# Kernel optimization log

Hardware: AMD Instinct MI355X
Metric: run time of the kernel (lower is better)

## Reference

```python
import jax, jax.numpy as jnp
import numpy as np

N, E, F_IN, C, H12, H3, NCLS = 10000, 160000, 50, 256, 4, 6, 121


def gat_conv(x, src, dst, W, a_src, a_dst, b, heads, out_ch, concat, n):
    # x: [n, f_in]; W: [f_in, heads*out_ch]; a_*: [heads, out_ch]; src/dst: [e]
    h = (x @ W).reshape(n, heads, out_ch)
    # per-edge attention logits, LeakyReLU(0.2) as in PyG GATConv
    alpha = jax.nn.leaky_relu((h * a_src).sum(-1)[src] + (h * a_dst).sum(-1)[dst], 0.2)  # [e, heads]
    # segment softmax over incoming edges of each destination node
    amax = jax.ops.segment_max(alpha, dst, num_segments=n)
    ex = jnp.exp(alpha - amax[dst])
    denom = jax.ops.segment_sum(ex, dst, num_segments=n)
    w = ex / (denom[dst] + 1e-16)
    out = jax.ops.segment_sum(h[src] * w[..., None], dst, num_segments=n)  # [n, heads, out_ch]
    out = out.reshape(n, heads * out_ch) if concat else out.mean(axis=1)
    return out + b


def setup_inputs() -> dict:
    key = jax.random.key(0)
    ks = jax.random.split(key, 22)
    s = 0.05
    nrm = lambda k, shp: jax.random.normal(k, shp, jnp.float32) * s
    D = C * H12  # 1024
    return {
        "x": jax.random.normal(ks[0], (N, F_IN), jnp.float32),
        "edge_index": jax.random.randint(ks[1], (2, E), 0, N, dtype=jnp.int32),
        "W1": nrm(ks[2], (F_IN, H12 * C)), "a_src1": nrm(ks[3], (H12, C)), "a_dst1": nrm(ks[4], (H12, C)), "b1": jnp.zeros((H12 * C,), jnp.float32),
        "lW1": nrm(ks[5], (F_IN, D)), "lb1": jnp.zeros((D,), jnp.float32),
        "W2": nrm(ks[6], (D, H12 * C)), "a_src2": nrm(ks[7], (H12, C)), "a_dst2": nrm(ks[8], (H12, C)), "b2": jnp.zeros((H12 * C,), jnp.float32),
        "lW2": nrm(ks[9], (D, D)), "lb2": jnp.zeros((D,), jnp.float32),
        "W3": nrm(ks[10], (D, H3 * NCLS)), "a_src3": nrm(ks[11], (H3, NCLS)), "a_dst3": nrm(ks[12], (H3, NCLS)), "b3": jnp.zeros((NCLS,), jnp.float32),
        "lW3": nrm(ks[13], (D, NCLS)), "lb3": jnp.zeros((NCLS,), jnp.float32),
    }


def reference(x, edge_index, W1, a_src1, a_dst1, b1, lW1, lb1,
              W2, a_src2, a_dst2, b2, lW2, lb2,
              W3, a_src3, a_dst3, b3, lW3, lb3):
    n = x.shape[0]
    loop = jnp.arange(n, dtype=edge_index.dtype)  # self loops (PyG default)
    src = jnp.concatenate([edge_index[0], loop])
    dst = jnp.concatenate([edge_index[1], loop])
    h = jax.nn.elu(gat_conv(x, src, dst, W1, a_src1, a_dst1, b1, H12, C, True, n) + x @ lW1 + lb1)
    h = jax.nn.elu(gat_conv(h, src, dst, W2, a_src2, a_dst2, b2, H12, C, True, n) + h @ lW2 + lb2)
    return gat_conv(h, src, dst, W3, a_src3, a_dst3, b3, H3, NCLS, False, n) + h @ lW3 + lb3
```

## Files before the change

kernel.cpp:

```cpp
#include <hip/hip_runtime.h>
#include <cstdint>
#include <cstddef>

#define NN 10000
#define EE 160000
#define EN_ (EE + NN)
#define MPAD 10112
#define MT 79
#define CAP 128

typedef short s16x8 __attribute__((ext_vector_type(8)));
typedef float f32x4 __attribute__((ext_vector_type(4)));
typedef unsigned short u16;
typedef unsigned char u8;

__device__ __forceinline__ u16 f2bf(float f) {
  uint32_t u = __float_as_uint(f);
  uint32_t r = (u + 0x7fffu + ((u >> 16) & 1u)) >> 16;
  return (u16)r;
}
__device__ __forceinline__ float b2f_lo(uint32_t p) { return __uint_as_float(p << 16); }
__device__ __forceinline__ float b2f_hi(uint32_t p) { return __uint_as_float(p & 0xffff0000u); }
__device__ __forceinline__ float lrelu02(float x) { return x > 0.f ? x : 0.2f * x; }
__device__ __forceinline__ float eluf(float x) { return x > 0.f ? x : (__expf(x) - 1.f); }
__device__ __forceinline__ u8 f2fp8(float v) {
  v = fminf(fmaxf(v, -448.f), 448.f);
  return (u8)(__builtin_amdgcn_cvt_pk_fp8_f32(v, v, 0, false) & 0xff);
}

__global__ void k_count(const int* __restrict__ ei, int* __restrict__ cnt) {
  int e = blockIdx.x * blockDim.x + threadIdx.x;
  if (e >= EN_) return;
  int d = (e < EE) ? ei[EE + e] : (e - EE);
  atomicAdd(&cnt[d], 1);
}

__global__ __launch_bounds__(1024) void k_scan(const int* __restrict__ cnt, int* __restrict__ off) {
  __shared__ int sums[1024];
  int t = threadIdx.x;
  const int per = (NN + 1023) / 1024;
  int base = t * per;
  int local = 0;
  for (int j = 0; j < per; ++j) {
    int idx = base + j;
    if (idx < NN) local += cnt[idx];
  }
  sums[t] = local;
  __syncthreads();
  for (int s = 1; s < 1024; s <<= 1) {
    int v = (t >= s) ? sums[t - s] : 0;
    __syncthreads();
    sums[t] += v;
    __syncthreads();
  }
  int run = (t == 0) ? 0 : sums[t - 1];
  for (int j = 0; j < per; ++j) {
    int idx = base + j;
    if (idx < NN) { off[idx] = run; run += cnt[idx]; }
  }
  if (t == 1023) off[NN] = EN_;
}

__global__ void k_fill(const int* __restrict__ ei, const int* __restrict__ off,
                       int* __restrict__ cursor, int* __restrict__ csr_src) {
  int e = blockIdx.x * blockDim.x + threadIdx.x;
  if (e >= EN_) return;
  int s, d;
  if (e < EE) { s = ei[e]; d = ei[EE + e]; } else { s = d = e - EE; }
  int p = atomicAdd(&cursor[d], 1);
  csr_src[off[d] + p] = s;
}

#define PREP_BLOCKS 3490
__global__ __launch_bounds__(256) void k_prep(
    const float* __restrict__ x, u16* __restrict__ xb,
    const float* __restrict__ W1, const float* __restrict__ lW1,
    const float* __restrict__ W2, const float* __restrict__ lW2,
    const float* __restrict__ W3, const float* __restrict__ lW3,
    u16* __restrict__ wtc1, u16* __restrict__ wtc2, u16* __restrict__ wtc3,
    const float* __restrict__ lb1, const float* __restrict__ lb2,
    const float* __restrict__ lb3, float* __restrict__ fb,
    u16* __restrict__ bufX, int* __restrict__ cnt) {
  int b = blockIdx.x, t = threadIdx.x;
  if (b < 768) {
    const float* W; u16* Bt; int K, N, Kpad, nb, kb;
    if (b < 16)       { W = W1;  Bt = wtc1;                       K = 50;   N = 1024; Kpad = 64;   nb = b;      kb = 0; }
    else if (b < 32)  { W = lW1; Bt = wtc1 + (size_t)1024 * 64;   K = 50;   N = 1024; Kpad = 64;   nb = b - 16; kb = 0; }
    else if (b < 288) { int r = b - 32;  W = W2;  Bt = wtc2;                         K = 1024; N = 1024; Kpad = 1024; nb = r & 15; kb = r >> 4; }
    else if (b < 544) { int r = b - 288; W = lW2; Bt = wtc2 + (size_t)1024 * 1024;   K = 1024; N = 1024; Kpad = 1024; nb = r & 15; kb = r >> 4; }
    else if (b < 736) { int r = b - 544; W = W3;  Bt = wtc3;                         K = 1024; N = 726;  Kpad = 1024; nb = r % 12; kb = r / 12; }
    else              { int r = b - 736; W = lW3; Bt = wtc3 + (size_t)768 * 1024;    K = 1024; N = 121;  Kpad = 1024; nb = r & 1;  kb = r >> 1; }
    __shared__ float tile[64][65];
    int kbase = kb * 64, nbase = nb * 64;
    int nl = t & 63, kl0 = t >> 6;
#pragma unroll
    for (int j = 0; j < 16; ++j) {
      int k = kbase + kl0 + j * 4, n = nbase + nl;
      tile[kl0 + j * 4][nl] = (k < K && n < N) ? W[(size_t)k * N + n] : 0.f;
    }
    __syncthreads();
    int nr = t >> 2, kc = (t & 3) * 16;
    uint32_t pk[8];
#pragma unroll
    for (int j = 0; j < 8; ++j) {
      pk[j] = (uint32_t)f2bf(tile[kc + 2 * j][nr]) | ((uint32_t)f2bf(tile[kc + 2 * j + 1][nr]) << 16);
    }
    uint4* dst = (uint4*)(Bt + (size_t)(nbase + nr) * Kpad + kbase + kc);
    dst[0] = make_uint4(pk[0], pk[1], pk[2], pk[3]);
    dst[1] = make_uint4(pk[4], pk[5], pk[6], pk[7]);
  } else if (b < 3296) {
    int idx = (b - 768) * 256 + t;
    if (idx < MPAD * 64) {
      int m = idx >> 6, k = idx & 63;
      xb[idx] = f2bf((m < NN && k < 50) ? x[m * 50 + k] : 0.f);
    }
  } else if (b < 3352) {
    int idx = (b - 3296) * 256 + t;
    ((uint4*)(bufX + (size_t)NN * 1024))[idx] = make_uint4(0, 0, 0, 0);
  } else if (b < 3470) {
    int idx = (b - 3352) * 256 + t;
    if (idx < 3 * NN + 1) cnt[idx] = 0;
  } else {
    int idx = (b - 3470) * 256 + t;
    if (idx < 4992) {
      float v = 0.f;
      if (idx < 2048)      { if (idx >= 1024) v = lb1[idx - 1024]; }
      else if (idx < 4096) { int j = idx - 2048; if (j >= 1024) v = lb2[j - 1024]; }
      else                 { int j = idx - 4096; if (j >= 768 && j < 889) v = lb3[j - 768]; }
      fb[idx] = v;
    }
  }
}

template <int OUT_S_BF16>
__global__ __launch_bounds__(256) void k_gemm_fused(
    const u16* __restrict__ A, const u16* __restrict__ Bt,
    const float* __restrict__ fbias,
    u8* __restrict__ outH, int ldH,
    void* __restrict__ outS, int ldS, int nsplit, int nrealS,
    int M, int Kpad, int NS) {
  __shared__ __align__(16) u16 lA[128 * 64];
  __shared__ __align__(16) u16 lB[128 * 64];
  int bid = blockIdx.x;
  int xcd = bid & 7, seq = bid >> 3;
  int nIdx = seq % NS, mloc = seq / NS;
  int mIdx = mloc * 8 + xcd;
  if (mIdx >= MT) return;
  int bm = mIdx * 128, bn = nIdx * 128;

  int t = threadIdx.x;
  int wave = t >> 6, lane = t & 63;
  int wm = (wave >> 1) * 64, wn = (wave & 1) * 64;

  f32x4 acc[4][4];
#pragma unroll
  for (int i = 0; i < 4; ++i)
#pragma unroll
    for (int j = 0; j < 4; ++j)
#pragma unroll
      for (int r = 0; r < 4; ++r) acc[i][j][r] = 0.f;

  int row = lane & 15, quad = lane >> 4;

  for (int k0 = 0; k0 < Kpad; k0 += 64) {
#pragma unroll
    for (int is = 0; is < 4; ++is) {
      int L = is * 256 + t;
      int m = L >> 3, c = L & 7;
      int j = c ^ (m & 7);
      const u16* gpA = A + (size_t)(bm + m) * Kpad + k0 + j * 8;
      const u16* gpB = Bt + (size_t)(bn + m) * Kpad + k0 + j * 8;
      u16* lpA = lA + (size_t)(is * 256 + wave * 64) * 8;
      u16* lpB = lB + (size_t)(is * 256 + wave * 64) * 8;
      __builtin_amdgcn_global_load_lds(
          (const __attribute__((address_space(1))) void*)gpA,
          (__attribute__((address_space(3))) void*)lpA, 16, 0, 0);
      __builtin_amdgcn_global_load_lds(
          (const __attribute__((address_space(1))) void*)gpB,
          (__attribute__((address_space(3))) void*)lpB, 16, 0, 0);
    }
    __syncthreads();

#pragma unroll
    for (int kk = 0; kk < 2; ++kk) {
      s16x8 af[4], bf[4];
#pragma unroll
      for (int mi = 0; mi < 4; ++mi) {
        int m = wm + mi * 16 + row;
        int c = (kk * 4 + quad) ^ (m & 7);
        af[mi] = *(const s16x8*)&lA[m * 64 + c * 8];
      }
#pragma unroll
      for (int ni = 0; ni < 4; ++ni) {
        int n = wn + ni * 16 + row;
        int c = (kk * 4 + quad) ^ (n & 7);
        bf[ni] = *(const s16x8*)&lB[n * 64 + c * 8];
      }
#pragma unroll
      for (int mi = 0; mi < 4; ++mi)
#pragma unroll
        for (int ni = 0; ni < 4; ++ni)
          acc[mi][ni] = __builtin_amdgcn_mfma_f32_16x16x32_bf16(af[mi], bf[ni], acc[mi][ni], 0, 0, 0);
    }
    __syncthreads();
  }

  int col = lane & 15, qr = (lane >> 4) * 4;
  bool isH = bn < nsplit;
#pragma unroll
  for (int mi = 0; mi < 4; ++mi) {
#pragma unroll
    for (int r = 0; r < 4; ++r) {
      int m = bm + wm + mi * 16 + qr + r;
      if (m >= M) continue;
#pragma unroll
      for (int ni = 0; ni < 4; ++ni) {
        int n = bn + wn + ni * 16 + col;
        float v = acc[mi][ni][r] + fbias[n];
        if (isH) {
          outH[(size_t)m * ldH + n] = f2fp8(v);
        } else {
          int c = n - nsplit;
          if (c < nrealS) {
            if (OUT_S_BF16) ((u16*)outS)[(size_t)m * ldS + c] = f2bf(v);
            else ((float*)outS)[(size_t)m * ldS + c] = v;
          }
        }
      }
    }
  }
}

__global__ void k_scores256(const u8* __restrict__ h, const float* __restrict__ a_src,
                            const float* __restrict__ a_dst, float* __restrict__ as_,
                            float* __restrict__ ad_) {
  int wid = (blockIdx.x * blockDim.x + threadIdx.x) >> 6;
  int lane = threadIdx.x & 63;
  if (wid >= NN * 4) return;
  int i = wid >> 2, hh = wid & 3;
  int pk = *(const int*)(h + (size_t)i * 1024 + hh * 256 + 4 * lane);
  float4 av = *(const float4*)(a_src + hh * 256 + 4 * lane);
  float4 dv = *(const float4*)(a_dst + hh * 256 + 4 * lane);
  float x0 = __builtin_amdgcn_cvt_f32_fp8(pk, 0);
  float x1 = __builtin_amdgcn_cvt_f32_fp8(pk, 1);
  float x2 = __builtin_amdgcn_cvt_f32_fp8(pk, 2);
  float x3 = __builtin_amdgcn_cvt_f32_fp8(pk, 3);
  float s1 = x0 * av.x + x1 * av.y + x2 * av.z + x3 * av.w;
  float s2 = x0 * dv.x + x1 * dv.y + x2 * dv.z + x3 * dv.w;
#pragma unroll
  for (int o = 32; o; o >>= 1) {
    s1 += __shfl_down(s1, o);
    s2 += __shfl_down(s2, o);
  }
  if (lane == 0) { as_[wid] = s1; ad_[wid] = s2; }
}

__global__ void k_scores(const u8* __restrict__ h, const float* __restrict__ a_src,
                         const float* __restrict__ a_dst, float* __restrict__ as_,
                         float* __restrict__ ad_, int H, int C, int ld) {
  int wid = (blockIdx.x * blockDim.x + threadIdx.x) >> 6;
  int lane = threadIdx.x & 63;
  if (wid >= NN * H) return;
  int i = wid / H, hh = wid - i * H;
  const u8* hp = h + (size_t)i * ld + hh * C;
  const float* sp = a_src + hh * C;
  const float* dp = a_dst + hh * C;
  float s1 = 0.f, s2 = 0.f;
  for (int c = lane; c < C; c += 64) {
    float v = __builtin_amdgcn_cvt_f32_fp8((int)hp[c], 0);
    s1 += v * sp[c];
    s2 += v * dp[c];
  }
#pragma unroll
  for (int o = 32; o; o >>= 1) {
    s1 += __shfl_down(s1, o);
    s2 += __shfl_down(s2, o);
  }
  if (lane == 0) { as_[wid] = s1; ad_[wid] = s2; }
}

__global__ __launch_bounds__(256) void k_agg_cat(
    const u8* __restrict__ h, const float* __restrict__ as_, const float* __restrict__ ad_,
    const int* __restrict__ off, const int* __restrict__ csr_src,
    const float* __restrict__ bias, const u16* __restrict__ skip, u16* __restrict__ outx) {
  const int F = 1024;
  int i = blockIdx.x, t = threadIdx.x;
  int start = off[i], end = off[i + 1];
  int wave = t >> 6, lane = t & 63;
  __shared__ int src_s[CAP];
  __shared__ float a_s[CAP][4];
  float4 adv = *(const float4*)(ad_ + (size_t)i * 4);
  float m_run = -1e30f, denom = 0.f;
  float acc0 = 0.f, acc1 = 0.f, acc2 = 0.f, acc3 = 0.f;
  for (int e0 = start; e0 < end; e0 += CAP) {
    int ne = min(CAP, end - e0);
    if (e0 > start) __syncthreads();
    if (t < ne) {
      int s = csr_src[e0 + t];
      src_s[t] = s;
      float4 av = *(const float4*)(as_ + (size_t)s * 4);
      a_s[t][0] = lrelu02(av.x + adv.x);
      a_s[t][1] = lrelu02(av.y + adv.y);
      a_s[t][2] = lrelu02(av.z + adv.z);
      a_s[t][3] = lrelu02(av.w + adv.w);
    }
    __syncthreads();
    float cm = -1e30f;
    for (int j = lane; j < ne; j += 64) cm = fmaxf(cm, a_s[j][wave]);
#pragma unroll
    for (int msk = 32; msk; msk >>= 1) cm = fmaxf(cm, __shfl_xor(cm, msk));
    float nm = fmaxf(m_run, cm);
    float sm = 0.f;
    for (int j = lane; j < ne; j += 64) {
      float e = __expf(a_s[j][wave] - nm);
      a_s[j][wave] = e;
      sm += e;
    }
#pragma unroll
    for (int msk = 32; msk; msk >>= 1) sm += __shfl_xor(sm, msk);
    float rs = __expf(m_run - nm);
    acc0 *= rs; acc1 *= rs; acc2 *= rs; acc3 *= rs;
    denom = denom * rs + sm;
    m_run = nm;
#pragma unroll 4
    for (int e = 0; e < ne; ++e) {
      int pk = *(const int*)(h + (size_t)src_s[e] * F + 4 * t);
      float ww = a_s[e][wave];
      acc0 += ww * __builtin_amdgcn_cvt_f32_fp8(pk, 0);
      acc1 += ww * __builtin_amdgcn_cvt_f32_fp8(pk, 1);
      acc2 += ww * __builtin_amdgcn_cvt_f32_fp8(pk, 2);
      acc3 += ww * __builtin_amdgcn_cvt_f32_fp8(pk, 3);
    }
  }
  float rdm = 1.f / (denom + 1e-16f);
  int ch = 4 * t;
  float4 bb = *(const float4*)(bias + ch);
  uint2 sk = *(const uint2*)(skip + (size_t)i * F + ch);
  u16 o0 = f2bf(eluf(acc0 * rdm + bb.x + b2f_lo(sk.x)));
  u16 o1 = f2bf(eluf(acc1 * rdm + bb.y + b2f_hi(sk.x)));
  u16 o2 = f2bf(eluf(acc2 * rdm + bb.z + b2f_lo(sk.y)));
  u16 o3 = f2bf(eluf(acc3 * rdm + bb.w + b2f_hi(sk.y)));
  uint2 ov;
  ov.x = (uint32_t)o0 | ((uint32_t)o1 << 16);
  ov.y = (uint32_t)o2 | ((uint32_t)o3 << 16);
  *(uint2*)(outx + (size_t)i * F + ch) = ov;
}

__global__ __launch_bounds__(256) void k_agg_mean(
    const u8* __restrict__ h, const float* __restrict__ as_, const float* __restrict__ ad_,
    const int* __restrict__ off, const int* __restrict__ csr_src,
    const float* __restrict__ bias, float* __restrict__ out) {
  const int H = 6, C = 121, FP = 768;
  int i = blockIdx.x, t = threadIdx.x;
  int start = off[i], end = off[i + 1];
  int wave = t >> 6, lane = t & 63;
  __shared__ int src_s[CAP];
  __shared__ float a_s[CAP][H];
  __shared__ float nm_s[H], sm_s[H];
  __shared__ float agg_s[FP];
  float adv[H];
  {
    float2 v0 = *(const float2*)(ad_ + (size_t)i * H);
    float2 v1 = *(const float2*)(ad_ + (size_t)i * H + 2);
    float2 v2 = *(const float2*)(ad_ + (size_t)i * H + 4);
    adv[0] = v0.x; adv[1] = v0.y; adv[2] = v1.x; adv[3] = v1.y; adv[4] = v2.x; adv[5] = v2.y;
  }
  int c0 = 4 * t;
  bool act = t < 192;
  int hd[4];
#pragma unroll
  for (int r = 0; r < 4; ++r) {
    int c = c0 + r;
    hd[r] = (act && c < 726) ? (c / C) : 0;
  }
  float acc[4] = {0.f, 0.f, 0.f, 0.f};
  float m_r[4] = {-1e30f, -1e30f, -1e30f, -1e30f};
  float d_r[4] = {0.f, 0.f, 0.f, 0.f};
  for (int e0 = start; e0 < end; e0 += CAP) {
    int ne = min(CAP, end - e0);
    if (e0 > start) __syncthreads();
    if (t < ne) {
      int s = csr_src[e0 + t];
      src_s[t] = s;
      float2 v0 = *(const float2*)(as_ + (size_t)s * H);
      float2 v1 = *(const float2*)(as_ + (size_t)s * H + 2);
      float2 v2 = *(const float2*)(as_ + (size_t)s * H + 4);
      a_s[t][0] = lrelu02(v0.x + adv[0]);
      a_s[t][1] = lrelu02(v0.y + adv[1]);
      a_s[t][2] = lrelu02(v1.x + adv[2]);
      a_s[t][3] = lrelu02(v1.y + adv[3]);
      a_s[t][4] = lrelu02(v2.x + adv[4]);
      a_s[t][5] = lrelu02(v2.y + adv[5]);
    }
    __syncthreads();
    for (int hh = wave; hh < H; hh += 4) {
      float cm = -1e30f;
      for (int j = lane; j < ne; j += 64) cm = fmaxf(cm, a_s[j][hh]);
#pragma unroll
      for (int msk = 32; msk; msk >>= 1) cm = fmaxf(cm, __shfl_xor(cm, msk));
      float sm = 0.f;
      for (int j = lane; j < ne; j += 64) {
        float e = __expf(a_s[j][hh] - cm);
        a_s[j][hh] = e;
        sm += e;
      }
#pragma unroll
      for (int msk = 32; msk; msk >>= 1) sm += __shfl_xor(sm, msk);
      if (lane == 0) { nm_s[hh] = cm; sm_s[hh] = sm; }
    }
    __syncthreads();
    if (act) {
      float rsn[4];
#pragma unroll
      for (int r = 0; r < 4; ++r) {
        float cm = nm_s[hd[r]];
        float nm = fmaxf(m_r[r], cm);
        float rs_old = __expf(m_r[r] - nm);
        float rs_new = __expf(cm - nm);
        acc[r] *= rs_old;
        d_r[r] = d_r[r] * rs_old + sm_s[hd[r]] * rs_new;
        m_r[r] = nm;
        rsn[r] = rs_new;
      }
#pragma unroll 4
      for (int e = 0; e < ne; ++e) {
        const u8* hp = h + (size_t)src_s[e] * FP;
        int pk = *(const int*)(hp + c0);
        acc[0] += rsn[0] * a_s[e][hd[0]] * __builtin_amdgcn_cvt_f32_fp8(pk, 0);
        acc[1] += rsn[1] * a_s[e][hd[1]] * __builtin_amdgcn_cvt_f32_fp8(pk, 1);
        acc[2] += rsn[2] * a_s[e][hd[2]] * __builtin_amdgcn_cvt_f32_fp8(pk, 2);
        acc[3] += rsn[3] * a_s[e][hd[3]] * __builtin_amdgcn_cvt_f32_fp8(pk, 3);
      }
    }
  }
  __syncthreads();
  if (act) {
#pragma unroll
    for (int r = 0; r < 4; ++r) agg_s[c0 + r] = acc[r] / (d_r[r] + 1e-16f);
  }
  __syncthreads();
  if (t < C) {
    float s = 0.f;
#pragma unroll
    for (int hh = 0; hh < H; ++hh) s += agg_s[hh * C + t];
    size_t idx = (size_t)i * C + t;
    out[idx] += s * (1.f / 6.f) + bias[t];
  }
}

extern "C" void kernel_launch(void* const* d_in, const int* in_sizes, int n_in,
                              void* d_out, int out_size, void* d_ws, size_t ws_size,
                              hipStream_t stream) {
  const float* x = (const float*)d_in[0];
  const int* ei = (const int*)d_in[1];
  const float* W1 = (const float*)d_in[2];
  const float* a_src1 = (const float*)d_in[3];
  const float* a_dst1 = (const float*)d_in[4];
  const float* b1 = (const float*)d_in[5];
  const float* lW1 = (const float*)d_in[6];
  const float* lb1 = (const float*)d_in[7];
  const float* W2 = (const float*)d_in[8];
  const float* a_src2 = (const float*)d_in[9];
  const float* a_dst2 = (const float*)d_in[10];
  const float* b2 = (const float*)d_in[11];
  const float* lW2 = (const float*)d_in[12];
  const float* lb2 = (const float*)d_in[13];
  const float* W3 = (const float*)d_in[14];
  const float* a_src3 = (const float*)d_in[15];
  const float* a_dst3 = (const float*)d_in[16];
  const float* b3 = (const float*)d_in[17];
  const float* lW3 = (const float*)d_in[18];
  const float* lb3 = (const float*)d_in[19];
  float* outp = (float*)d_out;

  char* ws = (char*)d_ws;
  size_t o = 0;
  auto alloc = [&](size_t bytes) { void* p = ws + o; o += (bytes + 255) & ~(size_t)255; return p; };
  u8* bufH8 = (u8*)alloc((size_t)MPAD * 1024);
  u16* bufX = (u16*)alloc((size_t)MPAD * 1024 * 2);
  u16* bufS = (u16*)alloc((size_t)NN * 1024 * 2);
  u16* xb16 = (u16*)alloc((size_t)MPAD * 64 * 2);
  u16* wtc1 = (u16*)alloc((size_t)2048 * 64 * 2);
  u16* wtc2 = (u16*)alloc((size_t)2048 * 1024 * 2);
  u16* wtc3 = (u16*)alloc((size_t)896 * 1024 * 2);
  float* fb12 = (float*)alloc((size_t)4992 * 4);
  float* fb1 = fb12;
  float* fb2 = fb12 + 2048;
  float* fb3 = fb12 + 4096;
  float* as_ = (float*)alloc((size_t)NN * 6 * 4);
  float* ad_ = (float*)alloc((size_t)NN * 6 * 4);
  int* cnt = (int*)alloc((size_t)(3 * NN + 1) * 4);
  int* offs = cnt + NN;
  int* cursor = offs + NN + 1;
  int* csr_src = (int*)alloc((size_t)EN_ * 4);

  k_prep<<<PREP_BLOCKS, 256, 0, stream>>>(x, xb16, W1, lW1, W2, lW2, W3, lW3,
                                          wtc1, wtc2, wtc3, lb1, lb2, lb3, fb12,
                                          bufX, cnt);
  int eb = (EN_ + 255) / 256;
  k_count<<<eb, 256, 0, stream>>>(ei, cnt);
  k_scan<<<1, 1024, 0, stream>>>(cnt, offs);
  k_fill<<<eb, 256, 0, stream>>>(ei, offs, cursor, csr_src);

  {
    k_gemm_fused<1><<<16 * 80, 256, 0, stream>>>(
        xb16, wtc1, fb1, bufH8, 1024, bufS, 1024, 1024, 1024, NN, 64, 16);
    k_scores256<<<10000, 256, 0, stream>>>(bufH8, a_src1, a_dst1, as_, ad_);
    k_agg_cat<<<NN, 256, 0, stream>>>(bufH8, as_, ad_, offs, csr_src, b1, bufS, bufX);
  }
  {
    k_gemm_fused<1><<<16 * 80, 256, 0, stream>>>(
        bufX, wtc2, fb2, bufH8, 1024, bufS, 1024, 1024, 1024, NN, 1024, 16);
    k_scores256<<<10000, 256, 0, stream>>>(bufH8, a_src2, a_dst2, as_, ad_);
    k_agg_cat<<<NN, 256, 0, stream>>>(bufH8, as_, ad_, offs, csr_src, b2, bufS, bufX);
  }
  {
    k_gemm_fused<0><<<7 * 80, 256, 0, stream>>>(
        bufX, wtc3, fb3, bufH8, 768, outp, 121, 768, 121, NN, 1024, 7);
    k_scores<<<(NN * 6 + 3) / 4, 256, 0, stream>>>(bufH8, a_src3, a_dst3, as_, ad_, 6, 121, 768);
    k_agg_mean<<<NN, 256, 0, stream>>>(bufH8, as_, ad_, offs, csr_src, b3, outp);
  }
}
```

Measured before the change: 416.9 us.

## Pack GEMM epilogue stores via lane shuffles and fold edge counting into prep

The GEMM epilogue now uses lane shuffles to gather four adjacent columns into one lane, so it writes packed 32-bit fp8 words and 64-bit bf16 words instead of scattered byte and short stores. Separately, the edge-count kernel is merged into the prep kernel, and the count buffers are cleared by a memset before prep runs. This aims to cut uncoalesced store traffic in every GEMM and to remove one kernel launch. The cost is extra shuffle instructions per output row and an added memset call.

```diff
diff --git a/kernel.cpp b/kernel.cpp
--- a/kernel.cpp
+++ b/kernel.cpp
@@ -26,13 +26,6 @@
 __device__ __forceinline__ u8 f2fp8(float v) {
   v = fminf(fmaxf(v, -448.f), 448.f);
   return (u8)(__builtin_amdgcn_cvt_pk_fp8_f32(v, v, 0, false) & 0xff);
-}
-
-__global__ void k_count(const int* __restrict__ ei, int* __restrict__ cnt) {
-  int e = blockIdx.x * blockDim.x + threadIdx.x;
-  if (e >= EN_) return;
-  int d = (e < EE) ? ei[EE + e] : (e - EE);
-  atomicAdd(&cnt[d], 1);
 }
 
 __global__ __launch_bounds__(1024) void k_scan(const int* __restrict__ cnt, int* __restrict__ off) {
@@ -71,7 +64,7 @@
   csr_src[off[d] + p] = s;
 }
 
-#define PREP_BLOCKS 3490
+#define PREP_BLOCKS 4037
 __global__ __launch_bounds__(256) void k_prep(
     const float* __restrict__ x, u16* __restrict__ xb,
     const float* __restrict__ W1, const float* __restrict__ lW1,
@@ -80,7 +73,7 @@
     u16* __restrict__ wtc1, u16* __restrict__ wtc2, u16* __restrict__ wtc3,
     const float* __restrict__ lb1, const float* __restrict__ lb2,
     const float* __restrict__ lb3, float* __restrict__ fb,
-    u16* __restrict__ bufX, int* __restrict__ cnt) {
+    u16* __restrict__ bufX, const int* __restrict__ ei, int* __restrict__ cnt) {
   int b = blockIdx.x, t = threadIdx.x;
   if (b < 768) {
     const float* W; u16* Bt; int K, N, Kpad, nb, kb;
@@ -117,17 +110,20 @@
   } else if (b < 3352) {
     int idx = (b - 3296) * 256 + t;
     ((uint4*)(bufX + (size_t)NN * 1024))[idx] = make_uint4(0, 0, 0, 0);
-  } else if (b < 3470) {
+  } else if (b < 3372) {
     int idx = (b - 3352) * 256 + t;
-    if (idx < 3 * NN + 1) cnt[idx] = 0;
-  } else {
-    int idx = (b - 3470) * 256 + t;
     if (idx < 4992) {
       float v = 0.f;
       if (idx < 2048)      { if (idx >= 1024) v = lb1[idx - 1024]; }
       else if (idx < 4096) { int j = idx - 2048; if (j >= 1024) v = lb2[j - 1024]; }
       else                 { int j = idx - 4096; if (j >= 768 && j < 889) v = lb3[j - 768]; }
       fb[idx] = v;
+    }
+  } else {
+    int e = (b - 3372) * 256 + t;
+    if (e < EN_) {
+      int d = (e < EE) ? ei[EE + e] : (e - EE);
+      atomicAdd(&cnt[d], 1);
     }
   }
 }
@@ -205,25 +201,71 @@
     __syncthreads();
   }
 
-  int col = lane & 15, qr = (lane >> 4) * 4;
+  int col16 = lane & 15, qr = (lane >> 4) * 4;
+  int qbase = lane & 48;
   bool isH = bn < nsplit;
-#pragma unroll
-  for (int mi = 0; mi < 4; ++mi) {
-#pragma unroll
-    for (int r = 0; r < 4; ++r) {
-      int m = bm + wm + mi * 16 + qr + r;
-      if (m >= M) continue;
-#pragma unroll
-      for (int ni = 0; ni < 4; ++ni) {
-        int n = bn + wn + ni * 16 + col;
-        float v = acc[mi][ni][r] + fbias[n];
-        if (isH) {
-          outH[(size_t)m * ldH + n] = f2fp8(v);
+  int srcs[4];
+#pragma unroll
+  for (int k = 0; k < 4; ++k) srcs[k] = qbase | ((4 * col16 + k) & 15);
+  int bsel = col16 >> 2;
+  if (isH) {
+#pragma unroll
+    for (int mi = 0; mi < 4; ++mi) {
+#pragma unroll
+      for (int r = 0; r < 4; ++r) {
+        int m = bm + wm + mi * 16 + qr + r;
+        float vc[4];
+#pragma unroll
+        for (int ni = 0; ni < 4; ++ni) {
+          float v = acc[mi][ni][r] + fbias[bn + wn + ni * 16 + col16];
+          vc[ni] = fminf(fmaxf(v, -448.f), 448.f);
+        }
+        uint32_t D = (uint32_t)__builtin_amdgcn_cvt_pk_fp8_f32(vc[0], vc[1], 0, false);
+        D = (uint32_t)__builtin_amdgcn_cvt_pk_fp8_f32(vc[2], vc[3], D, true);
+        uint32_t outw = 0;
+#pragma unroll
+        for (int k = 0; k < 4; ++k) {
+          uint32_t rk = (uint32_t)__shfl((int)D, srcs[k]);
+          outw |= ((rk >> (8 * bsel)) & 0xffu) << (8 * k);
+        }
+        if (m < M)
+          *(uint32_t*)(outH + (size_t)m * ldH + (bn + wn + 4 * col16)) = outw;
+      }
+    }
+  } else {
+#pragma unroll
+    for (int mi = 0; mi < 4; ++mi) {
+#pragma unroll
+      for (int r = 0; r < 4; ++r) {
+        int m = bm + wm + mi * 16 + qr + r;
+        float vv[4];
+#pragma unroll
+        for (int ni = 0; ni < 4; ++ni)
+          vv[ni] = acc[mi][ni][r] + fbias[bn + wn + ni * 16 + col16];
+        if (OUT_S_BF16) {
+          uint32_t D0 = (uint32_t)f2bf(vv[0]) | ((uint32_t)f2bf(vv[1]) << 16);
+          uint32_t D1 = (uint32_t)f2bf(vv[2]) | ((uint32_t)f2bf(vv[3]) << 16);
+          uint32_t lo = 0, hi = 0;
+#pragma unroll
+          for (int k = 0; k < 4; ++k) {
+            uint32_t ra = (uint32_t)__shfl((int)D0, srcs[k]);
+            uint32_t rb = (uint32_t)__shfl((int)D1, srcs[k]);
+            uint32_t rw = (bsel & 2) ? rb : ra;
+            uint32_t h16 = (rw >> (16 * (bsel & 1))) & 0xffffu;
+            if (k < 2) lo |= h16 << (16 * k);
+            else hi |= h16 << (16 * (k - 2));
+          }
+          if (m < M) {
+            int cg = bn + wn + 4 * col16 - nsplit;
+            uint2 ov; ov.x = lo; ov.y = hi;
+            *(uint2*)((u16*)outS + (size_t)m * ldS + cg) = ov;
+          }
         } else {
-          int c = n - nsplit;
-          if (c < nrealS) {
-            if (OUT_S_BF16) ((u16*)outS)[(size_t)m * ldS + c] = f2bf(v);
-            else ((float*)outS)[(size_t)m * ldS + c] = v;
+#pragma unroll
+          for (int ni = 0; ni < 4; ++ni) {
+            int c = bn + wn + ni * 16 + col16 - nsplit;
+            if (m < M && c < nrealS)
+              ((float*)outS)[(size_t)m * ldS + c] = vv[ni];
           }
         }
       }
@@ -494,13 +536,12 @@
   int* cursor = offs + NN + 1;
   int* csr_src = (int*)alloc((size_t)EN_ * 4);
 
+  hipMemsetAsync(cnt, 0, (size_t)(3 * NN + 1) * 4, stream);
   k_prep<<<PREP_BLOCKS, 256, 0, stream>>>(x, xb16, W1, lW1, W2, lW2, W3, lW3,
                                           wtc1, wtc2, wtc3, lb1, lb2, lb3, fb12,
-                                          bufX, cnt);
-  int eb = (EN_ + 255) / 256;
-  k_count<<<eb, 256, 0, stream>>>(ei, cnt);
+                                          bufX, ei, cnt);
   k_scan<<<1, 1024, 0, stream>>>(cnt, offs);
-  k_fill<<<eb, 256, 0, stream>>>(ei, offs, cursor, csr_src);
+  k_fill<<<(EN_ + 255) / 256, 256, 0, stream>>>(ei, offs, cursor, csr_src);
 
   {
     k_gemm_fused<1><<<16 * 80, 256, 0, stream>>>(
```

Measured after the change: 388.2 us. -6.9%, faster.
